# Optimization experiments

Measured on AMD Instinct MI355X. Metric: run time of the kernel, lower is better.

The kernel has to match this reference:

```python
import jax, jax.numpy as jnp
import numpy as np

N, E = 100000, 1000000
HID, EDGE_D, DIST_D, TIME_D, EXTRA = 128, 64, 64, 128, 3
HEADS = 1 + EXTRA
IN_CH = 2 * HID + EDGE_D + DIST_D


def setup_inputs() -> dict:
    key = jax.random.key(0)
    ks = jax.random.split(key, 16)
    inp = {
        "h": jax.random.normal(ks[0], (N, HID), jnp.float32),
        "pos": jax.random.normal(ks[1], (N, 3), jnp.float32),
        "edge_attr": jax.random.normal(ks[2], (E, EDGE_D), jnp.float32),
        "dist": jax.random.normal(ks[3], (E, DIST_D), jnp.float32),
        "time_emb": jax.random.normal(ks[4], (E, TIME_D), jnp.float32),
        "adj_extra": jax.random.uniform(ks[5], (E, EXTRA), jnp.float32),
        # params
        "W_time": jax.random.normal(ks[6], (TIME_D, 2 * HID), jnp.float32) / np.sqrt(TIME_D),
        "b_time": jnp.zeros((2 * HID,), jnp.float32),
        "W_in": jax.random.normal(ks[7], (IN_CH, HID), jnp.float32) / np.sqrt(IN_CH),
        "b_in": jnp.zeros((HID,), jnp.float32),
        "W1": jax.random.normal(ks[8], (HID, HID), jnp.float32) / np.sqrt(HID),
        "b1": jnp.zeros((HID,), jnp.float32),
        "W2": jax.random.normal(ks[9], (HID, HEADS), jnp.float32) / np.sqrt(HID),
        "coors_scale": jnp.full((1,), 0.01, jnp.float32),
        "edge_index": jax.random.randint(ks[10], (2, E), 0, N, jnp.int32),
    }
    return inp


def _layernorm(x, eps=1e-6):
    mu = jnp.mean(x, axis=-1, keepdims=True)
    var = jnp.var(x, axis=-1, keepdims=True)
    return (x - mu) * jax.lax.rsqrt(var + eps)


def reference(h, pos, edge_attr, dist, time_emb, adj_extra,
              W_time, b_time, W_in, b_in, W1, b1, W2, coors_scale,
              edge_index):
    row, col = edge_index[0], edge_index[1]
    # gather node features per edge: [E, 2H+edge+dist]
    h_input = jnp.concatenate([h[row], h[col], edge_attr, dist], axis=1)
    # CoorsNorm(scale_init=0.01)
    coord_diff = pos[row] - pos[col]                       # [E, 3]
    norm = jnp.linalg.norm(coord_diff, axis=-1, keepdims=True)
    coord_diff = coord_diff / jnp.maximum(norm, 1e-8) * coors_scale
    # time conditioning: SiLU -> Linear -> (shift, scale)
    t = jax.nn.silu(time_emb) @ W_time + b_time            # [E, 2H]
    shift, scale = jnp.split(t, 2, axis=1)
    inv = _layernorm(h_input @ W_in + b_in)                # [E, H]
    inv = inv * (1.0 + scale) + shift                      # modulate
    # coord MLP -> per-head scalar, tanh-bounded
    inv = jnp.tanh(jax.nn.silu(inv @ W1 + b1) @ W2)        # [E, heads]
    adjs = jnp.concatenate([jnp.ones((adj_extra.shape[0], 1), inv.dtype), adj_extra], axis=-1)
    inv = jnp.mean(inv * adjs, axis=-1, keepdims=True)     # [E, 1]
    trans = coord_diff * inv                               # [E, 3]
    agg = jax.ops.segment_sum(trans, row, num_segments=pos.shape[0])
    return pos + agg
```

## Files before the change

kernel.cpp:

```cpp
#include <hip/hip_runtime.h>
#include <hip/hip_bf16.h>

#define E_EDGES 1000000
#define N_NODES 100000

typedef __attribute__((ext_vector_type(8))) short bf16x8;
typedef __attribute__((ext_vector_type(4))) float f32x4;

#define WAITV(N) asm volatile("s_waitcnt vmcnt(" #N ")" ::: "memory")
#define WAITL()  asm volatile("s_waitcnt lgkmcnt(0)" ::: "memory")
#define BAR()    __builtin_amdgcn_s_barrier()

__device__ __forceinline__ short f2bf(float f) {
    union { __bf16 b; short s; } u;
    u.b = (__bf16)f;
    return u.s;
}
__device__ __forceinline__ bf16x8 pack8(float4 a, float4 b) {
    bf16x8 r;
    r[0]=f2bf(a.x); r[1]=f2bf(a.y); r[2]=f2bf(a.z); r[3]=f2bf(a.w);
    r[4]=f2bf(b.x); r[5]=f2bf(b.y); r[6]=f2bf(b.z); r[7]=f2bf(b.w);
    return r;
}
__device__ __forceinline__ float4 ld4(const float* p) {
    return *reinterpret_cast<const float4*>(p);
}
__device__ __forceinline__ float silu1(float x) { return x / (1.f + __expf(-x)); }
__device__ __forceinline__ float tanh1(float x) {
    float e = __expf(2.f * x);
    return 1.f - 2.f / (e + 1.f);
}
__device__ __forceinline__ float bf2f(unsigned short u) {
    return __uint_as_float(((unsigned)u) << 16);
}

__device__ __forceinline__ void stage_frag(const short* gsrc, short* ldst) {
    __builtin_amdgcn_global_load_lds(
        (const __attribute__((address_space(1))) void*)gsrc,
        (__attribute__((address_space(3))) void*)ldst, 16, 0, 0);
}

__device__ __forceinline__ int tswz(int row, int colS) {
    return (row * 64 + colS) ^ ((row & 7) << 3);
}

__global__ void pack_weights_f(const float* __restrict__ Wt,
                               const float* __restrict__ Win,
                               const float* __restrict__ W1,
                               const float* __restrict__ W2,
                               short* __restrict__ ws)
{
    int gid = blockIdx.x * 256 + threadIdx.x;
    if (gid >= 196 * 512) return;
    int frag = gid >> 9, within = gid & 511;
    int l = within >> 3, j = within & 7;
    int lg = l >> 4, ln = l & 15;
    int krow = (lg << 3) + j;
    float v;
    if (frag < 32) {
        int ks = frag >> 3, nt = frag & 7;
        v = Win[(256 + ks * 32 + krow) * 128 + nt * 16 + ln];
    } else if (frag < 96) {
        int t = frag - 32, ch = t >> 3, sub = t & 7;
        int jj = sub >> 2, ks = sub & 3;
        int jcol = (ch < 4) ? (8 + 2 * ch + jj) : (2 * (ch - 4) + jj);
        v = Wt[(ks * 32 + krow) * 256 + jcol * 16 + ln];
    } else if (frag < 128) {
        int t = frag - 96, ch = t >> 3, sub = t & 7;
        int nt = 2 * ch + (sub >> 2), ks = sub & 3;
        v = W1[(ks * 32 + krow) * 128 + nt * 16 + ln];
    } else if (frag < 132) {
        int ks = frag - 128;
        v = (ln < 4) ? W2[(ks * 32 + krow) * 4 + ln] : 0.0f;
    } else {
        int q = frag - 132;
        int ntc = q >> 2, ks = q & 3;
        int base = (ntc < 8) ? 0 : 128;
        v = Win[(base + ks * 32 + krow) * 128 + (ntc & 7) * 16 + ln];
    }
    ws[gid] = f2bf(v);
}

__global__ __launch_bounds__(256)
void hpre_kernel(const float* __restrict__ h, const short* __restrict__ ws,
                 short* __restrict__ hp)
{
    const int tid = threadIdx.x;
    const int w   = tid >> 6;
    const int l   = tid & 63;
    const int ln  = l & 15;
    const int lg  = l >> 4;
    const int kb  = lg << 3;
    const int nb  = blockIdx.x * 64 + w * 16;
    const int nm  = min(nb + ln, N_NODES - 1);

    bf16x8 af[4];
    #pragma unroll
    for (int ks = 0; ks < 4; ++ks)
        af[ks] = pack8(ld4(h + (long)nm * 128 + ks*32 + kb),
                       ld4(h + (long)nm * 128 + ks*32 + kb + 4));
    const short* wsp = ws + 132 * 512;
    #pragma unroll
    for (int ntc = 0; ntc < 16; ++ntc) {
        f32x4 acc = (f32x4){0.f,0.f,0.f,0.f};
        #pragma unroll
        for (int ks = 0; ks < 4; ++ks) {
            bf16x8 b = *reinterpret_cast<const bf16x8*>(&wsp[(ntc*4+ks)*512 + l*8]);
            acc = __builtin_amdgcn_mfma_f32_16x16x32_bf16(af[ks], b, acc, 0, 0, 0);
        }
        #pragma unroll
        for (int r = 0; r < 4; ++r) {
            int node = nb + (lg<<2) + r;
            if (node < N_NODES)
                hp[(long)node * 256 + ntc*16 + ln] = f2bf(acc[r]);
        }
    }
}

__global__ __launch_bounds__(256, 3)
void edge_kernel_f(const float* __restrict__ pos,
                   const float* __restrict__ ea,
                   const float* __restrict__ dst_f,
                   const float* __restrict__ temb,
                   const float* __restrict__ adj,
                   const float* __restrict__ btime,
                   const float* __restrict__ bin,
                   const float* __restrict__ b1,
                   const float* __restrict__ cscale,
                   const int*   __restrict__ ei,
                   const short* __restrict__ ws,
                   const unsigned short* __restrict__ hp,
                   float* __restrict__ out)
{
    __shared__ __align__(16) short Wb[3][4096];
    __shared__ float sBias[512];

    const int tid = threadIdx.x;
    const int w   = tid >> 6;
    const int l   = tid & 63;
    const int ln  = l & 15;
    const int lg  = l >> 4;
    const int kb  = lg << 3;
    const int e0w = blockIdx.x * 64 + w * 16;
    const int em  = e0w + ln;

    const int ir = ei[em];
    const int ic = ei[E_EDGES + em];

    #pragma unroll
    for (int i = 0; i < 2; ++i) {
        int idx = tid + i * 256;
        float v = (idx < 128) ? bin[idx] : (idx < 256) ? b1[idx - 128] : btime[idx - 256];
        sBias[idx] = v;
    }
    WAITL();

    #define STAGE8(p) { \
        const short* g_ = ws + (p) * 4096 + (w*2) * 512 + l * 8; \
        short* d_ = &Wb[(p) % 3][(w*2) * 512]; \
        stage_frag(g_, d_); \
        stage_frag(g_ + 512, d_ + 512); }
    #define STAGEW2() { \
        stage_frag(ws + 16 * 4096 + w * 512 + l * 8, &Wb[1][w * 512]); }

    int irg[4], icg[4];
    #pragma unroll
    for (int r = 0; r < 4; ++r) {
        irg[r] = __shfl(ir, (lg<<2) + r);
        icg[r] = __shfl(ic, (lg<<2) + r);
    }

    unsigned short ga[32], gb[32];
    #pragma unroll
    for (int r = 0; r < 4; ++r)
        #pragma unroll
        for (int nt = 0; nt < 8; ++nt) {
            ga[r*8+nt] = hp[(long)irg[r]*256 + (nt<<4) + ln];
            gb[r*8+nt] = hp[(long)icg[r]*256 + 128 + (nt<<4) + ln];
        }
    float4 tf[8];
    #pragma unroll
    for (int k2 = 0; k2 < 4; ++k2) {
        const float* q = (k2 < 2) ? (ea    + (long)em*64 + k2*32 + kb)
                                  : (dst_f + (long)em*64 + (k2-2)*32 + kb);
        tf[2*k2]   = ld4(q);
        tf[2*k2+1] = ld4(q + 4);
    }
    STAGE8(0);
    STAGE8(1);
    WAITV(4);

    f32x4 accX[8];
    #pragma unroll
    for (int r = 0; r < 4; ++r)
        #pragma unroll
        for (int nt = 0; nt < 8; ++nt)
            accX[nt][r] = bf2f(ga[r*8+nt]) + bf2f(gb[r*8+nt]);
    bf16x8 af_a[4];
    #pragma unroll
    for (int k2 = 0; k2 < 4; ++k2) af_a[k2] = pack8(tf[2*k2], tf[2*k2+1]);

    #pragma unroll
    for (int c = 0; c < 4; ++c) {
        if (c == 3) { WAITV(10); } else { WAITV(2); }
        BAR();
        STAGE8(c + 2);
        if (c == 2) {
            #pragma unroll
            for (int k2 = 0; k2 < 4; ++k2) {
                tf[2*k2]   = ld4(temb + (long)em * 128 + k2*32 + kb);
                tf[2*k2+1] = ld4(temb + (long)em * 128 + k2*32 + kb + 4);
            }
        }
        {
            const short* wb = &Wb[c % 3][0];
            #pragma unroll
            for (int nt = 0; nt < 8; ++nt) {
                bf16x8 b = *reinterpret_cast<const bf16x8*>(&wb[nt*512 + l*8]);
                accX[nt] = __builtin_amdgcn_mfma_f32_16x16x32_bf16(af_a[c], b, accX[nt], 0, 0, 0);
            }
        }
    }

    #pragma unroll
    for (int nt = 0; nt < 8; ++nt) {
        float bv = sBias[(nt<<4) + ln];
        #pragma unroll
        for (int r = 0; r < 4; ++r) accX[nt][r] += bv;
    }
    #pragma unroll
    for (int r = 0; r < 4; ++r) {
        float p = 0.f, q = 0.f;
        #pragma unroll
        for (int nt = 0; nt < 8; ++nt) { float x = accX[nt][r]; p += x; q += x*x; }
        #pragma unroll
        for (int d2 = 1; d2 < 16; d2 <<= 1) { p += __shfl_xor(p, d2); q += __shfl_xor(q, d2); }
        float mean = p * 0.0078125f;
        float var  = q * 0.0078125f - mean * mean;
        float rstd = rsqrtf(var + 1e-6f);
        #pragma unroll
        for (int nt = 0; nt < 8; ++nt)
            accX[nt][r] = (accX[nt][r] - mean) * rstd;
    }

    WAITV(2);
    bf16x8 ttf[4];
    #pragma unroll
    for (int k2 = 0; k2 < 4; ++k2) {
        float4 va = tf[2*k2], vb = tf[2*k2+1];
        va.x=silu1(va.x); va.y=silu1(va.y); va.z=silu1(va.z); va.w=silu1(va.w);
        vb.x=silu1(vb.x); vb.y=silu1(vb.y); vb.z=silu1(vb.z); vb.w=silu1(vb.w);
        ttf[k2] = pack8(va, vb);
    }

    #pragma unroll
    for (int t = 0; t < 8; ++t) {
        WAITV(2);
        BAR();
        STAGE8(6 + t);
        {
            const short* wb = &Wb[(4 + t) % 3][0];
            #pragma unroll
            for (int jj = 0; jj < 2; ++jj) {
                f32x4 tt = (f32x4){0.f,0.f,0.f,0.f};
                #pragma unroll
                for (int ks = 0; ks < 4; ++ks) {
                    bf16x8 b = *reinterpret_cast<const bf16x8*>(&wb[(jj*4+ks)*512 + l*8]);
                    tt = __builtin_amdgcn_mfma_f32_16x16x32_bf16(ttf[ks], b, tt, 0, 0, 0);
                }
                if (t < 4) {
                    const int jx = 2*t + jj;
                    float bsc = sBias[384 + (jx<<4) + ln];
                    #pragma unroll
                    for (int r = 0; r < 4; ++r) accX[jx][r] *= (1.f + tt[r] + bsc);
                } else {
                    const int jx = 2*(t-4) + jj;
                    float bsh = sBias[256 + (jx<<4) + ln];
                    #pragma unroll
                    for (int r = 0; r < 4; ++r) accX[jx][r] += tt[r] + bsh;
                }
            }
        }
    }

    short* tbW = &Wb[2][w * 1024];
    bf16x8 iaf[4];
    WAITL();
    BAR();
    #pragma unroll
    for (int hpx = 0; hpx < 2; ++hpx) {
        #pragma unroll
        for (int nt4 = 0; nt4 < 4; ++nt4) {
            const int nt = hpx*4 + nt4;
            #pragma unroll
            for (int r = 0; r < 4; ++r)
                tbW[tswz((lg<<2) + r, (nt4<<4) + ln)] = f2bf(accX[nt][r]);
        }
        #pragma unroll
        for (int k2 = 0; k2 < 2; ++k2)
            iaf[hpx*2 + k2] = *reinterpret_cast<const bf16x8*>(&tbW[tswz(ln, (k2<<5) + kb)]);
    }
    WAITL();

    f32x4 accY[8];
    #pragma unroll
    for (int i = 0; i < 8; ++i) accY[i] = (f32x4){0.f,0.f,0.f,0.f};
    #pragma unroll
    for (int u = 0; u < 4; ++u) {
        if (u < 3) { WAITV(2); } else { WAITV(1); }
        BAR();
        if (u == 0)      { STAGE8(14); }
        else if (u == 1) { STAGE8(15); }
        else if (u == 2) { STAGEW2(); }
        {
            const short* wb = &Wb[(12 + u) % 3][0];
            #pragma unroll
            for (int s = 0; s < 2; ++s) {
                const int nt = 2*u + s;
                #pragma unroll
                for (int ks = 0; ks < 4; ++ks) {
                    bf16x8 b = *reinterpret_cast<const bf16x8*>(&wb[(s*4+ks)*512 + l*8]);
                    accY[nt] = __builtin_amdgcn_mfma_f32_16x16x32_bf16(iaf[ks], b, accY[nt], 0, 0, 0);
                }
            }
        }
    }

    bf16x8 yaf[4];
    WAITL();
    BAR();
    #pragma unroll
    for (int hpx = 0; hpx < 2; ++hpx) {
        #pragma unroll
        for (int nt4 = 0; nt4 < 4; ++nt4) {
            const int nt = hpx*4 + nt4;
            float bv = sBias[128 + (nt<<4) + ln];
            #pragma unroll
            for (int r = 0; r < 4; ++r)
                tbW[tswz((lg<<2) + r, (nt4<<4) + ln)] = f2bf(silu1(accY[nt][r] + bv));
        }
        #pragma unroll
        for (int k2 = 0; k2 < 2; ++k2)
            yaf[hpx*2 + k2] = *reinterpret_cast<const bf16x8*>(&tbW[tswz(ln, (k2<<5) + kb)]);
    }

    WAITV(0);
    BAR();
    f32x4 accZ = (f32x4){0.f,0.f,0.f,0.f};
    {
        const short* wb = &Wb[1][0];
        #pragma unroll
        for (int ks = 0; ks < 4; ++ks) {
            bf16x8 b = *reinterpret_cast<const bf16x8*>(&wb[ks*512 + l*8]);
            accZ = __builtin_amdgcn_mfma_f32_16x16x32_bf16(yaf[ks], b, accZ, 0, 0, 0);
        }
    }

    {
        float dx = pos[ir*3+0] - pos[ic*3+0];
        float dy = pos[ir*3+1] - pos[ic*3+1];
        float dz = pos[ir*3+2] - pos[ic*3+2];
        float a0 = adj[em*3+0], a1 = adj[em*3+1], a2 = adj[em*3+2];
        float nrm = sqrtf(dx*dx + dy*dy + dz*dz);
        float sc  = cscale[0] / fmaxf(nrm, 1e-8f);
        float cdx = dx * sc, cdy = dy * sc, cdz = dz * sc;
        #pragma unroll
        for (int r = 0; r < 4; ++r) {
            const int m = (lg<<2) + r;
            float z  = tanh1(accZ[r]);
            float w0 = __shfl(a0, m), w1 = __shfl(a1, m), w2 = __shfl(a2, m);
            int   irm  = __shfl(ir, m);
            float cdxm = __shfl(cdx, m), cdym = __shfl(cdy, m), cdzm = __shfl(cdz, m);
            float wt = (ln == 0) ? 1.0f : (ln == 1 ? w0 : (ln == 2 ? w1 : (ln == 3 ? w2 : 0.0f)));
            float v = z * wt;
            v += __shfl_xor(v, 1);
            v += __shfl_xor(v, 2);
            float s = v * 0.25f;
            if (ln < 3) {
                float cdc = (ln == 0) ? cdxm : (ln == 1 ? cdym : cdzm);
                atomicAdd(&out[(long)irm*3 + ln], cdc * s);
            }
        }
    }
    #undef STAGE8
    #undef STAGEW2
}

__global__ void pack_weights_fb(const float* __restrict__ Wt,
                                const float* __restrict__ Win,
                                const float* __restrict__ W1,
                                const float* __restrict__ W2,
                                short* __restrict__ ws)
{
    int gid = blockIdx.x * 256 + threadIdx.x;
    if (gid >= 196 * 512) return;
    int frag = gid >> 9, within = gid & 511;
    int l = within >> 3, j = within & 7;
    int lg = l >> 4, ln = l & 15;
    int krow = (lg << 3) + j;
    float v;
    if (frag < 96) {
        int cs = frag >> 3, nt = frag & 7;
        int seg = cs >> 2, ks = cs & 3;
        int base = (seg == 0) ? 256 : (seg == 1) ? 0 : 128;
        int k = base + ks * 32 + krow;
        v = Win[k * 128 + nt * 16 + ln];
    } else if (frag < 160) {
        int t = frag - 96, ch = t >> 3, sub = t & 7;
        int jj = sub >> 2, ks = sub & 3;
        int jcol = (ch < 4) ? (8 + 2 * ch + jj) : (2 * (ch - 4) + jj);
        int k = ks * 32 + krow;
        v = Wt[k * 256 + jcol * 16 + ln];
    } else if (frag < 192) {
        int t = frag - 160, ch = t >> 3, sub = t & 7;
        int nt = 2 * ch + (sub >> 2), ks = sub & 3;
        int k = ks * 32 + krow;
        v = W1[k * 128 + nt * 16 + ln];
    } else {
        int ks = frag - 192;
        int k = ks * 32 + krow;
        v = (ln < 4) ? W2[k * 4 + ln] : 0.0f;
    }
    ws[gid] = f2bf(v);
}

__global__ void h_pack_kernel(const float* __restrict__ h, short* __restrict__ hbf) {
    long i = (long)(blockIdx.x * 256 + threadIdx.x) * 8;
    if (i >= (long)N_NODES * 128) return;
    float4 a = ld4(h + i), b = ld4(h + i + 4);
    *reinterpret_cast<bf16x8*>(hbf + i) = pack8(a, b);
}

template<bool HBF>
__global__ __launch_bounds__(256, 3)
void edge_kernel_fb(const float* __restrict__ h,
                    const short* __restrict__ hbf,
                    const float* __restrict__ pos,
                    const float* __restrict__ ea,
                    const float* __restrict__ dst_f,
                    const float* __restrict__ temb,
                    const float* __restrict__ adj,
                    const float* __restrict__ btime,
                    const float* __restrict__ bin,
                    const float* __restrict__ b1,
                    const float* __restrict__ cscale,
                    const int*   __restrict__ ei,
                    const short* __restrict__ ws,
                    float* __restrict__ out)
{
    __shared__ __align__(16) short Wb[3][4096];
    __shared__ float sBias[512];

    const int tid = threadIdx.x;
    const int w   = tid >> 6;
    const int l   = tid & 63;
    const int ln  = l & 15;
    const int lg  = l >> 4;
    const int kb  = lg << 3;
    const int e0w = blockIdx.x * 64 + w * 16;
    const int em  = e0w + ln;

    const int ir = ei[em];
    const int ic = ei[E_EDGES + em];

    #pragma unroll
    for (int i = 0; i < 2; ++i) {
        int idx = tid + i * 256;
        float v = (idx < 128) ? bin[idx] : (idx < 256) ? b1[idx - 128] : btime[idx - 256];
        sBias[idx] = v;
    }
    WAITL();

    #define STAGE8(p) { \
        const short* g_ = ws + (p) * 4096 + (w*2) * 512 + l * 8; \
        short* d_ = &Wb[(p) % 3][(w*2) * 512]; \
        stage_frag(g_, d_); \
        stage_frag(g_ + 512, d_ + 512); }
    #define STAGEW2() { \
        stage_frag(ws + 24 * 4096 + w * 512 + l * 8, &Wb[0][w * 512]); }

    float4 tf[8];
    #pragma unroll
    for (int k2 = 0; k2 < 4; ++k2) {
        const float* q = (k2 < 2) ? (ea    + (long)em*64 + k2*32 + kb)
                                  : (dst_f + (long)em*64 + (k2-2)*32 + kb);
        tf[2*k2]   = ld4(q);
        tf[2*k2+1] = ld4(q + 4);
    }
    bf16x8 af_b[4];
    if (HBF) {
        #pragma unroll
        for (int k2 = 0; k2 < 4; ++k2)
            af_b[k2] = *reinterpret_cast<const bf16x8*>(hbf + (long)ir * 128 + k2*32 + kb);
    } else {
        #pragma unroll
        for (int k2 = 0; k2 < 4; ++k2)
            af_b[k2] = pack8(ld4(h + (long)ir*128 + k2*32 + kb),
                             ld4(h + (long)ir*128 + k2*32 + kb + 4));
    }
    STAGE8(0);
    STAGE8(1);
    if (HBF) { WAITV(8); } else { WAITV(4); }
    bf16x8 af_a[4];
    #pragma unroll
    for (int k2 = 0; k2 < 4; ++k2) af_a[k2] = pack8(tf[2*k2], tf[2*k2+1]);

    f32x4 accX[8];
    #pragma unroll
    for (int i = 0; i < 8; ++i) accX[i] = (f32x4){0.f,0.f,0.f,0.f};
    bf16x8 af_c[4];

    #pragma unroll
    for (int c = 0; c < 12; ++c) {
        if (HBF) {
            if (c == 4 || c == 5) { WAITV(6); } else { WAITV(2); }
        } else {
            if (c == 4 || c == 5) { WAITV(10); } else { WAITV(2); }
        }
        BAR();
        if (c == 11) {
            #pragma unroll
            for (int k2 = 0; k2 < 4; ++k2) {
                tf[2*k2]   = ld4(temb + (long)em * 128 + k2*32 + kb);
                tf[2*k2+1] = ld4(temb + (long)em * 128 + k2*32 + kb + 4);
            }
        }
        STAGE8(c + 2);
        if (c == 3) {
            if (HBF) {
                #pragma unroll
                for (int k2 = 0; k2 < 4; ++k2)
                    af_c[k2] = *reinterpret_cast<const bf16x8*>(hbf + (long)ic * 128 + k2*32 + kb);
            } else {
                #pragma unroll
                for (int k2 = 0; k2 < 4; ++k2)
                    af_c[k2] = pack8(ld4(h + (long)ic*128 + k2*32 + kb),
                                     ld4(h + (long)ic*128 + k2*32 + kb + 4));
            }
        }
        {
            const int ks = c & 3;
            const bf16x8 a_use = (c < 4) ? af_a[ks] : (c < 8) ? af_b[ks] : af_c[ks];
            const short* wb = &Wb[c % 3][0];
            #pragma unroll
            for (int nt = 0; nt < 8; ++nt) {
                bf16x8 b = *reinterpret_cast<const bf16x8*>(&wb[nt*512 + l*8]);
                accX[nt] = __builtin_amdgcn_mfma_f32_16x16x32_bf16(a_use, b, accX[nt], 0, 0, 0);
            }
        }
    }

    #pragma unroll
    for (int nt = 0; nt < 8; ++nt) {
        float bv = sBias[(nt<<4) + ln];
        #pragma unroll
        for (int r = 0; r < 4; ++r) accX[nt][r] += bv;
    }
    #pragma unroll
    for (int r = 0; r < 4; ++r) {
        float p = 0.f, q = 0.f;
        #pragma unroll
        for (int nt = 0; nt < 8; ++nt) { float x = accX[nt][r]; p += x; q += x*x; }
        #pragma unroll
        for (int d2 = 1; d2 < 16; d2 <<= 1) { p += __shfl_xor(p, d2); q += __shfl_xor(q, d2); }
        float mean = p * 0.0078125f;
        float var  = q * 0.0078125f - mean * mean;
        float rstd = rsqrtf(var + 1e-6f);
        #pragma unroll
        for (int nt = 0; nt < 8; ++nt)
            accX[nt][r] = (accX[nt][r] - mean) * rstd;
    }

    WAITV(2);
    bf16x8 ttf[4];
    #pragma unroll
    for (int k2 = 0; k2 < 4; ++k2) {
        float4 va = tf[2*k2], vb = tf[2*k2+1];
        va.x=silu1(va.x); va.y=silu1(va.y); va.z=silu1(va.z); va.w=silu1(va.w);
        vb.x=silu1(vb.x); vb.y=silu1(vb.y); vb.z=silu1(vb.z); vb.w=silu1(vb.w);
        ttf[k2] = pack8(va, vb);
    }

    #pragma unroll
    for (int t = 0; t < 8; ++t) {
        WAITV(2);
        BAR();
        STAGE8(14 + t);
        {
            const short* wb = &Wb[(12 + t) % 3][0];
            #pragma unroll
            for (int jj = 0; jj < 2; ++jj) {
                f32x4 tt = (f32x4){0.f,0.f,0.f,0.f};
                #pragma unroll
                for (int ks = 0; ks < 4; ++ks) {
                    bf16x8 b = *reinterpret_cast<const bf16x8*>(&wb[(jj*4+ks)*512 + l*8]);
                    tt = __builtin_amdgcn_mfma_f32_16x16x32_bf16(ttf[ks], b, tt, 0, 0, 0);
                }
                if (t < 4) {
                    const int jx = 2*t + jj;
                    float bsc = sBias[384 + (jx<<4) + ln];
                    #pragma unroll
                    for (int r = 0; r < 4; ++r) accX[jx][r] *= (1.f + tt[r] + bsc);
                } else {
                    const int jx = 2*(t-4) + jj;
                    float bsh = sBias[256 + (jx<<4) + ln];
                    #pragma unroll
                    for (int r = 0; r < 4; ++r) accX[jx][r] += tt[r] + bsh;
                }
            }
        }
    }

    short* tbW = &Wb[1][w * 1024];
    bf16x8 iaf[4];
    WAITL();
    BAR();
    #pragma unroll
    for (int hpx = 0; hpx < 2; ++hpx) {
        #pragma unroll
        for (int nt4 = 0; nt4 < 4; ++nt4) {
            const int nt = hpx*4 + nt4;
            #pragma unroll
            for (int r = 0; r < 4; ++r)
                tbW[tswz((lg<<2) + r, (nt4<<4) + ln)] = f2bf(accX[nt][r]);
        }
        #pragma unroll
        for (int k2 = 0; k2 < 2; ++k2)
            iaf[hpx*2 + k2] = *reinterpret_cast<const bf16x8*>(&tbW[tswz(ln, (k2<<5) + kb)]);
    }
    WAITL();

    f32x4 accY[8];
    #pragma unroll
    for (int i = 0; i < 8; ++i) accY[i] = (f32x4){0.f,0.f,0.f,0.f};
    #pragma unroll
    for (int u = 0; u < 4; ++u) {
        if (u < 3) { WAITV(2); } else { WAITV(1); }
        BAR();
        if (u < 2)       { STAGE8(22 + u); }
        else if (u == 2) { STAGEW2(); }
        {
            const short* wb = &Wb[(20 + u) % 3][0];
            #pragma unroll
            for (int s = 0; s < 2; ++s) {
                const int nt = 2*u + s;
                #pragma unroll
                for (int ks = 0; ks < 4; ++ks) {
                    bf16x8 b = *reinterpret_cast<const bf16x8*>(&wb[(s*4+ks)*512 + l*8]);
                    accY[nt] = __builtin_amdgcn_mfma_f32_16x16x32_bf16(iaf[ks], b, accY[nt], 0, 0, 0);
                }
            }
        }
    }

    bf16x8 yaf[4];
    WAITL();
    BAR();
    #pragma unroll
    for (int hpx = 0; hpx < 2; ++hpx) {
        #pragma unroll
        for (int nt4 = 0; nt4 < 4; ++nt4) {
            const int nt = hpx*4 + nt4;
            float bv = sBias[128 + (nt<<4) + ln];
            #pragma unroll
            for (int r = 0; r < 4; ++r)
                tbW[tswz((lg<<2) + r, (nt4<<4) + ln)] = f2bf(silu1(accY[nt][r] + bv));
        }
        #pragma unroll
        for (int k2 = 0; k2 < 2; ++k2)
            yaf[hpx*2 + k2] = *reinterpret_cast<const bf16x8*>(&tbW[tswz(ln, (k2<<5) + kb)]);
    }

    WAITV(0);
    BAR();
    f32x4 accZ = (f32x4){0.f,0.f,0.f,0.f};
    {
        const short* wb = &Wb[0][0];
        #pragma unroll
        for (int ks = 0; ks < 4; ++ks) {
            bf16x8 b = *reinterpret_cast<const bf16x8*>(&wb[ks*512 + l*8]);
            accZ = __builtin_amdgcn_mfma_f32_16x16x32_bf16(yaf[ks], b, accZ, 0, 0, 0);
        }
    }

    {
        float dx = pos[ir*3+0] - pos[ic*3+0];
        float dy = pos[ir*3+1] - pos[ic*3+1];
        float dz = pos[ir*3+2] - pos[ic*3+2];
        float a0 = adj[em*3+0], a1 = adj[em*3+1], a2 = adj[em*3+2];
        float nrm = sqrtf(dx*dx + dy*dy + dz*dz);
        float sc  = cscale[0] / fmaxf(nrm, 1e-8f);
        float cdx = dx * sc, cdy = dy * sc, cdz = dz * sc;
        #pragma unroll
        for (int r = 0; r < 4; ++r) {
            const int m = (lg<<2) + r;
            float z  = tanh1(accZ[r]);
            float w0 = __shfl(a0, m), w1 = __shfl(a1, m), w2 = __shfl(a2, m);
            int   irm  = __shfl(ir, m);
            float cdxm = __shfl(cdx, m), cdym = __shfl(cdy, m), cdzm = __shfl(cdz, m);
            float wt = (ln == 0) ? 1.0f : (ln == 1 ? w0 : (ln == 2 ? w1 : (ln == 3 ? w2 : 0.0f)));
            float v = z * wt;
            v += __shfl_xor(v, 1);
            v += __shfl_xor(v, 2);
            float s = v * 0.25f;
            if (ln < 3) {
                float cdc = (ln == 0) ? cdxm : (ln == 1 ? cdym : cdzm);
                atomicAdd(&out[(long)irm*3 + ln], cdc * s);
            }
        }
    }
    #undef STAGE8
    #undef STAGEW2
}

extern "C" void kernel_launch(void* const* d_in, const int* in_sizes, int n_in,
                              void* d_out, int out_size, void* d_ws, size_t ws_size,
                              hipStream_t stream) {
    const float* h     = (const float*)d_in[0];
    const float* pos   = (const float*)d_in[1];
    const float* ea    = (const float*)d_in[2];
    const float* dist  = (const float*)d_in[3];
    const float* temb  = (const float*)d_in[4];
    const float* adj   = (const float*)d_in[5];
    const float* Wt    = (const float*)d_in[6];
    const float* bt    = (const float*)d_in[7];
    const float* Win   = (const float*)d_in[8];
    const float* bin   = (const float*)d_in[9];
    const float* W1    = (const float*)d_in[10];
    const float* b1    = (const float*)d_in[11];
    const float* W2    = (const float*)d_in[12];
    const float* cs    = (const float*)d_in[13];
    const int*   ei    = (const int*)d_in[14];
    float*       out   = (float*)d_out;
    short*       ws    = (short*)d_ws;

    const size_t WF_SHORTS = 196 * 512;
    const size_t HP_SHORTS = (size_t)N_NODES * 256;
    const size_t HB_SHORTS = (size_t)N_NODES * 128;
    const bool factored = ws_size >= (WF_SHORTS + HP_SHORTS) * sizeof(short);

    hipMemcpyAsync(out, pos, (size_t)out_size * sizeof(float),
                   hipMemcpyDeviceToDevice, stream);

    if (factored) {
        short* hp = ws + WF_SHORTS;
        pack_weights_f<<<(196*512 + 255) / 256, 256, 0, stream>>>(Wt, Win, W1, W2, ws);
        hpre_kernel<<<(N_NODES + 63) / 64, 256, 0, stream>>>(h, ws, hp);
        edge_kernel_f<<<E_EDGES / 64, 256, 0, stream>>>(
            pos, ea, dist, temb, adj, bt, bin, b1, cs, ei, ws,
            (const unsigned short*)hp, out);
    } else {
        const bool use_hbf = ws_size >= (WF_SHORTS + HB_SHORTS) * sizeof(short);
        short* hbf = ws + WF_SHORTS;
        pack_weights_fb<<<(196*512 + 255) / 256, 256, 0, stream>>>(Wt, Win, W1, W2, ws);
        if (use_hbf) {
            h_pack_kernel<<<(int)(HB_SHORTS / 8 / 256), 256, 0, stream>>>(h, hbf);
            edge_kernel_fb<true><<<E_EDGES / 64, 256, 0, stream>>>(
                h, hbf, pos, ea, dist, temb, adj, bt, bin, b1, cs, ei, ws, out);
        } else {
            edge_kernel_fb<false><<<E_EDGES / 64, 256, 0, stream>>>(
                h, hbf, pos, ea, dist, temb, adj, bt, bin, b1, cs, ei, ws, out);
        }
    }
}
```

Measured before the change: 525.9 us.

## Switch weight staging to double-buffered 16-fragment chunks with fewer barriers

Weights were staged into LDS through three buffers of 8 fragments each. They now go through two buffers of 16 fragments, which halves the number of stage/barrier rounds in the input projection, time-modulation and W1 phases. The temb prefetch and the W2 slot are rescheduled to match the new buffer layout. In exchange, per-block LDS use grows, and most waits now drain all outstanding memory operations (vmcnt 0), which may reduce overlap between weight loads and MFMA work.

Result: no change. 526.3 us (+0.1%).

```diff
diff --git a/kernel.cpp b/kernel.cpp
--- a/kernel.cpp
+++ b/kernel.cpp
@@ -132,7 +132,7 @@
                    const unsigned short* __restrict__ hp,
                    float* __restrict__ out)
 {
-    __shared__ __align__(16) short Wb[3][4096];
+    __shared__ __align__(16) short Wb[2][8192];
     __shared__ float sBias[512];
 
     const int tid = threadIdx.x;
@@ -155,13 +155,15 @@
     }
     WAITL();
 
-    #define STAGE8(p) { \
-        const short* g_ = ws + (p) * 4096 + (w*2) * 512 + l * 8; \
-        short* d_ = &Wb[(p) % 3][(w*2) * 512]; \
+    #define STAGE16(C) { \
+        const short* g_ = ws + (C) * 8192 + (w*4) * 512 + l * 8; \
+        short* d_ = &Wb[(C) & 1][(w*4) * 512]; \
         stage_frag(g_, d_); \
-        stage_frag(g_ + 512, d_ + 512); }
+        stage_frag(g_ + 512, d_ + 512); \
+        stage_frag(g_ + 1024, d_ + 1024); \
+        stage_frag(g_ + 1536, d_ + 1536); }
     #define STAGEW2() { \
-        stage_frag(ws + 16 * 4096 + w * 512 + l * 8, &Wb[1][w * 512]); }
+        stage_frag(ws + 128 * 512 + w * 512 + l * 8, &Wb[0][w * 512]); }
 
     int irg[4], icg[4];
     #pragma unroll
@@ -186,9 +188,9 @@
         tf[2*k2]   = ld4(q);
         tf[2*k2+1] = ld4(q + 4);
     }
-    STAGE8(0);
-    STAGE8(1);
-    WAITV(4);
+    STAGE16(0);
+    STAGE16(1);
+    WAITV(8);
 
     f32x4 accX[8];
     #pragma unroll
@@ -200,28 +202,37 @@
     #pragma unroll
     for (int k2 = 0; k2 < 4; ++k2) af_a[k2] = pack8(tf[2*k2], tf[2*k2+1]);
 
-    #pragma unroll
-    for (int c = 0; c < 4; ++c) {
-        if (c == 3) { WAITV(10); } else { WAITV(2); }
-        BAR();
-        STAGE8(c + 2);
-        if (c == 2) {
-            #pragma unroll
-            for (int k2 = 0; k2 < 4; ++k2) {
-                tf[2*k2]   = ld4(temb + (long)em * 128 + k2*32 + kb);
-                tf[2*k2+1] = ld4(temb + (long)em * 128 + k2*32 + kb + 4);
-            }
-        }
-        {
-            const short* wb = &Wb[c % 3][0];
+    WAITV(4);
+    BAR();
+    {
+        const short* wb = &Wb[0][0];
+        #pragma unroll
+        for (int ksl = 0; ksl < 2; ++ksl)
             #pragma unroll
             for (int nt = 0; nt < 8; ++nt) {
-                bf16x8 b = *reinterpret_cast<const bf16x8*>(&wb[nt*512 + l*8]);
-                accX[nt] = __builtin_amdgcn_mfma_f32_16x16x32_bf16(af_a[c], b, accX[nt], 0, 0, 0);
-            }
-        }
-    }
-
+                bf16x8 b = *reinterpret_cast<const bf16x8*>(&wb[(ksl*8+nt)*512 + l*8]);
+                accX[nt] = __builtin_amdgcn_mfma_f32_16x16x32_bf16(af_a[ksl], b, accX[nt], 0, 0, 0);
+            }
+    }
+
+    WAITV(0);
+    BAR();
+    #pragma unroll
+    for (int k2 = 0; k2 < 4; ++k2) {
+        tf[2*k2]   = ld4(temb + (long)em * 128 + k2*32 + kb);
+        tf[2*k2+1] = ld4(temb + (long)em * 128 + k2*32 + kb + 4);
+    }
+    STAGE16(2);
+    {
+        const short* wb = &Wb[1][0];
+        #pragma unroll
+        for (int ksl = 0; ksl < 2; ++ksl)
+            #pragma unroll
+            for (int nt = 0; nt < 8; ++nt) {
+                bf16x8 b = *reinterpret_cast<const bf16x8*>(&wb[(ksl*8+nt)*512 + l*8]);
+                accX[nt] = __builtin_amdgcn_mfma_f32_16x16x32_bf16(af_a[2+ksl], b, accX[nt], 0, 0, 0);
+            }
+    }
     #pragma unroll
     for (int nt = 0; nt < 8; ++nt) {
         float bv = sBias[(nt<<4) + ln];
@@ -242,8 +253,7 @@
         for (int nt = 0; nt < 8; ++nt)
             accX[nt][r] = (accX[nt][r] - mean) * rstd;
     }
-
-    WAITV(2);
+    WAITV(4);
     bf16x8 ttf[4];
     #pragma unroll
     for (int k2 = 0; k2 < 4; ++k2) {
@@ -254,18 +264,20 @@
     }
 
     #pragma unroll
-    for (int t = 0; t < 8; ++t) {
-        WAITV(2);
+    for (int tc = 0; tc < 4; ++tc) {
+        WAITV(0);
         BAR();
-        STAGE8(6 + t);
-        {
-            const short* wb = &Wb[(4 + t) % 3][0];
+        STAGE16(3 + tc);
+        const short* wb = &Wb[tc & 1][0];
+        #pragma unroll
+        for (int tl = 0; tl < 2; ++tl) {
+            const int t = 2*tc + tl;
             #pragma unroll
             for (int jj = 0; jj < 2; ++jj) {
                 f32x4 tt = (f32x4){0.f,0.f,0.f,0.f};
                 #pragma unroll
                 for (int ks = 0; ks < 4; ++ks) {
-                    bf16x8 b = *reinterpret_cast<const bf16x8*>(&wb[(jj*4+ks)*512 + l*8]);
+                    bf16x8 b = *reinterpret_cast<const bf16x8*>(&wb[(tl*8 + jj*4 + ks)*512 + l*8]);
                     tt = __builtin_amdgcn_mfma_f32_16x16x32_bf16(ttf[ks], b, tt, 0, 0, 0);
                 }
                 if (t < 4) {
@@ -283,7 +295,7 @@
         }
     }
 
-    short* tbW = &Wb[2][w * 1024];
+    short* tbW = &Wb[1][w * 2048];
     bf16x8 iaf[4];
     WAITL();
     BAR();
@@ -305,25 +317,40 @@
     f32x4 accY[8];
     #pragma unroll
     for (int i = 0; i < 8; ++i) accY[i] = (f32x4){0.f,0.f,0.f,0.f};
-    #pragma unroll
-    for (int u = 0; u < 4; ++u) {
-        if (u < 3) { WAITV(2); } else { WAITV(1); }
-        BAR();
-        if (u == 0)      { STAGE8(14); }
-        else if (u == 1) { STAGE8(15); }
-        else if (u == 2) { STAGEW2(); }
-        {
-            const short* wb = &Wb[(12 + u) % 3][0];
+    WAITV(0);
+    BAR();
+    STAGE16(7);
+    {
+        const short* wb = &Wb[0][0];
+        #pragma unroll
+        for (int ul = 0; ul < 2; ++ul)
             #pragma unroll
             for (int s = 0; s < 2; ++s) {
-                const int nt = 2*u + s;
+                const int nt = 2*ul + s;
                 #pragma unroll
                 for (int ks = 0; ks < 4; ++ks) {
-                    bf16x8 b = *reinterpret_cast<const bf16x8*>(&wb[(s*4+ks)*512 + l*8]);
+                    bf16x8 b = *reinterpret_cast<const bf16x8*>(&wb[(ul*8 + s*4 + ks)*512 + l*8]);
                     accY[nt] = __builtin_amdgcn_mfma_f32_16x16x32_bf16(iaf[ks], b, accY[nt], 0, 0, 0);
                 }
             }
-        }
+    }
+
+    WAITV(0);
+    BAR();
+    STAGEW2();
+    {
+        const short* wb = &Wb[1][0];
+        #pragma unroll
+        for (int ul = 0; ul < 2; ++ul)
+            #pragma unroll
+            for (int s = 0; s < 2; ++s) {
+                const int nt = 4 + 2*ul + s;
+                #pragma unroll
+                for (int ks = 0; ks < 4; ++ks) {
+                    bf16x8 b = *reinterpret_cast<const bf16x8*>(&wb[(ul*8 + s*4 + ks)*512 + l*8]);
+                    accY[nt] = __builtin_amdgcn_mfma_f32_16x16x32_bf16(iaf[ks], b, accY[nt], 0, 0, 0);
+                }
+            }
     }
 
     bf16x8 yaf[4];
@@ -348,7 +375,7 @@
     BAR();
     f32x4 accZ = (f32x4){0.f,0.f,0.f,0.f};
     {
-        const short* wb = &Wb[1][0];
+        const short* wb = &Wb[0][0];
         #pragma unroll
         for (int ks = 0; ks < 4; ++ks) {
             bf16x8 b = *reinterpret_cast<const bf16x8*>(&wb[ks*512 + l*8]);
@@ -382,7 +409,7 @@
             }
         }
     }
-    #undef STAGE8
+    #undef STAGE16
     #undef STAGEW2
 }
 
```
